# Optimization experiments

Measured on AMD Instinct MI355X. Metric: run time of the kernel, lower is better.

## Reference

```python
import jax, jax.numpy as jnp
import numpy as np

NG, ND = 50000, 20000
EG, ED = 300000, 150000
FG = FD = 256
H = 256
FC = 2048
B = 65536
EPS = 1e-5


def _lrelu(x):
    return jnp.where(x >= 0, x, 0.01 * x)


def _bn(x, g, b):
    # BatchNorm1d in training mode: biased batch stats over the node dim
    m = x.mean(axis=0)
    v = ((x - m) ** 2).mean(axis=0)
    return (x - m) * jax.lax.rsqrt(v + EPS) * g + b


def _gconv(x, edge_index, Wr, br, Ws, n_nodes):
    # PyG GraphConv: out = lin_rel(sum_{j->i} x_j) + lin_root(x_i)
    src, dst = edge_index[0], edge_index[1]
    agg = jax.ops.segment_sum(x[src], dst, num_segments=n_nodes)  # [N, in]
    return agg @ Wr + br + x @ Ws


def setup_inputs() -> dict:
    key = jax.random.key(0)
    ks = iter(jax.random.split(key, 64))
    d = {}
    d["gene_x"] = jax.random.normal(next(ks), (NG, FG), jnp.float32)
    d["disease_x"] = jax.random.normal(next(ks), (ND, FD), jnp.float32)
    d["gene_edge_index"] = jax.random.randint(next(ks), (2, EG), 0, NG, jnp.int32)
    d["disease_edge_index"] = jax.random.randint(next(ks), (2, ED), 0, ND, jnp.int32)
    d["batch_idx"] = jax.random.randint(next(ks), (B, 2), 0, ND, jnp.int32)

    def lin(fin, fout):
        s = 1.0 / np.sqrt(fin)
        W = jax.random.uniform(next(ks), (fin, fout), jnp.float32, -s, s)
        b = jax.random.uniform(next(ks), (fout,), jnp.float32, -s, s)
        return W, b

    for p, fin in (("g", FG), ("d", FD)):
        for i in range(3):
            f = fin if i == 0 else H
            Wr, br = lin(f, H)
            Ws, _ = lin(f, H)
            d[f"{p}{i}_Wr"], d[f"{p}{i}_br"], d[f"{p}{i}_Ws"] = Wr, br, Ws
            d[f"bn{p}{i}_g"] = jnp.ones((H,), jnp.float32)
            d[f"bn{p}{i}_b"] = jnp.zeros((H,), jnp.float32)
    d["lin1_W"], d["lin1_b"] = lin(2 * H, FC)
    d["lin2_W"], d["lin2_b"] = lin(FC, FC // 2)
    d["lin3_W"], d["lin3_b"] = lin(FC // 2, FC // 4)
    d["lin4_W"], d["lin4_b"] = lin(FC // 4, 2)
    return d


def reference(gene_x, disease_x, gene_edge_index, disease_edge_index, batch_idx,
              g0_Wr, g0_br, g0_Ws, g1_Wr, g1_br, g1_Ws, g2_Wr, g2_br, g2_Ws,
              d0_Wr, d0_br, d0_Ws, d1_Wr, d1_br, d1_Ws, d2_Wr, d2_br, d2_Ws,
              bng0_g, bng0_b, bng1_g, bng1_b, bng2_g, bng2_b,
              bnd0_g, bnd0_b, bnd1_g, bnd1_b, bnd2_g, bnd2_b,
              lin1_W, lin1_b, lin2_W, lin2_b, lin3_W, lin3_b, lin4_W, lin4_b):
    # gene tower
    g0 = _bn(_lrelu(_gconv(gene_x, gene_edge_index, g0_Wr, g0_br, g0_Ws, NG)), bng0_g, bng0_b)
    g1 = _bn(_lrelu(_gconv(g0, gene_edge_index, g1_Wr, g1_br, g1_Ws, NG)), bng1_g, bng1_b)
    g2 = _bn(_lrelu(_gconv(g1, gene_edge_index, g2_Wr, g2_br, g2_Ws, NG)), bng2_g, bng2_b)
    gene_out = 0.7 * g0 + 0.2 * g1 + 0.1 * g2
    # disease tower
    h0 = _bn(_lrelu(_gconv(disease_x, disease_edge_index, d0_Wr, d0_br, d0_Ws, ND)), bnd0_g, bnd0_b)
    h1 = _bn(_lrelu(_gconv(h0, disease_edge_index, d1_Wr, d1_br, d1_Ws, ND)), bnd1_g, bnd1_b)
    h2 = _bn(_lrelu(_gconv(h1, disease_edge_index, d2_Wr, d2_br, d2_Ws, ND)), bnd2_g, bnd2_b)
    dis_out = 0.7 * h0 + 0.2 * h1 + 0.1 * h2
    # pair gather + MLP head (dropout is identity in eval)
    x = jnp.concatenate([gene_out[batch_idx[:, 0]], dis_out[batch_idx[:, 1]]], axis=1)
    x = _lrelu(x @ lin1_W + lin1_b)
    x = _lrelu(x @ lin2_W + lin2_b)
    x = _lrelu(x @ lin3_W + lin3_b)
    return x @ lin4_W + lin4_b
```

## Files before the change

kernel.cpp:

```cpp
#include <hip/hip_runtime.h>
#include <hip/hip_bf16.h>
#include <cstdint>
#include <cstddef>

#define N_G 50000
#define N_D 20000
#define E_G 300000
#define E_D 150000
#define BATCH 65536

typedef _Float16 f16;
typedef _Float16 f16x8 __attribute__((ext_vector_type(8)));
typedef _Float16 f16x4 __attribute__((ext_vector_type(4)));
typedef float f32x4 __attribute__((ext_vector_type(4)));

__device__ __forceinline__ float clampf(float v) {
    return fminf(fmaxf(v, -60000.f), 60000.f);
}

__device__ __forceinline__ void gl_lds16(const void* g, void* l) {
    __builtin_amdgcn_global_load_lds(
        (const __attribute__((address_space(1))) unsigned int*)g,
        (__attribute__((address_space(3))) unsigned int*)l, 16, 0, 0);
}

__global__ __launch_bounds__(256) void gemm_f16(
    const f16* __restrict__ A,
    const int* __restrict__ bidx,
    const f16* __restrict__ geneT, const f16* __restrict__ disT, int rowBase,
    const f16* __restrict__ Bt, const float* __restrict__ bias,
    f16* __restrict__ C, int M, int N, int K, int relu, int CB, int RB,
    const float* __restrict__ W4, float* __restrict__ outF)
{
    alignas(16) __shared__ f16 sA[128 * 64];
    alignas(16) __shared__ f16 sB[128 * 64];
    const int t = threadIdx.x;
    const int w = t >> 6, l = t & 63;
    const int wm = w >> 1, wn = w & 1;
    const int q = l >> 4, lr = l & 15;

    int flat = blockIdx.x;
    int cb, rb;
    if ((RB & 7) == 0) {
        int x = flat & 7, idx = flat >> 3;
        int Sx = RB >> 3;
        cb = idx % CB;
        rb = x * Sx + idx / CB;
    } else {
        cb = flat % CB;
        rb = flat / CB;
    }
    const int mBase = rb * 128, nBase = cb * 128;

    const int subrow = l >> 3;
    const int c = l & 7;
    const char* pA[4];
    const char* pD[4];
    const char* pB[4];
    const bool fused = (bidx != nullptr);
    const bool concat = (!fused && disT != nullptr);
    const bool twoSrc = fused || concat;
#pragma unroll
    for (int j = 0; j < 4; j++) {
        int seg = j * 4 + w;
        int lrow = seg * 8 + subrow;
        int coff = ((c ^ (lrow & 7)) << 4);
        if (fused) {
            int rg = rowBase + mBase + lrow;
            int gi = bidx[2 * rg], di = bidx[2 * rg + 1];
            pA[j] = (const char*)geneT + (size_t)gi * 512 + coff;
            pD[j] = (const char*)disT + (size_t)di * 512 + coff;
        } else if (concat) {
            int arow = mBase + lrow; if (arow > M - 1) arow = M - 1;
            pA[j] = (const char*)geneT + (size_t)arow * 512 + coff;
            pD[j] = (const char*)disT + (size_t)arow * 512 + coff;
        } else {
            int arow = mBase + lrow; if (arow > M - 1) arow = M - 1;
            pA[j] = (const char*)A + (size_t)arow * K * 2 + coff;
            pD[j] = nullptr;
        }
        int brow = nBase + lrow; if (brow > N - 1) brow = N - 1;
        pB[j] = (const char*)Bt + (size_t)brow * K * 2 + coff;
    }

    f32x4 acc[4][4] = {};

    for (int k0 = 0; k0 < K; k0 += 64) {
        __syncthreads();
#pragma unroll
        for (int j = 0; j < 4; j++) {
            int seg = j * 4 + w;
            const char* srcA;
            if (twoSrc)
                srcA = (k0 < 256) ? (pA[j] + (size_t)k0 * 2) : (pD[j] + (size_t)(k0 - 256) * 2);
            else
                srcA = pA[j] + (size_t)k0 * 2;
            gl_lds16(srcA, sA + seg * 512);
            gl_lds16(pB[j] + (size_t)k0 * 2, sB + seg * 512);
        }
        __syncthreads();
        f16x8 a0[4], a1[4], b0[4], b1[4];
#pragma unroll
        for (int i = 0; i < 4; i++) {
            int r = wm * 64 + i * 16 + lr;
            int rs = r * 64;
            int x0 = (q ^ (r & 7)) << 3;
            int x1 = ((4 + q) ^ (r & 7)) << 3;
            a0[i] = *(const f16x8*)(sA + rs + x0);
            a1[i] = *(const f16x8*)(sA + rs + x1);
        }
#pragma unroll
        for (int jj = 0; jj < 4; jj++) {
            int r = wn * 64 + jj * 16 + lr;
            int rs = r * 64;
            int x0 = (q ^ (r & 7)) << 3;
            int x1 = ((4 + q) ^ (r & 7)) << 3;
            b0[jj] = *(const f16x8*)(sB + rs + x0);
            b1[jj] = *(const f16x8*)(sB + rs + x1);
        }
#pragma unroll
        for (int i = 0; i < 4; i++)
#pragma unroll
            for (int jj = 0; jj < 4; jj++) {
                acc[i][jj] = __builtin_amdgcn_mfma_f32_16x16x32_f16(a0[i], b0[jj], acc[i][jj], 0, 0, 0);
                acc[i][jj] = __builtin_amdgcn_mfma_f32_16x16x32_f16(a1[i], b1[jj], acc[i][jj], 0, 0, 0);
            }
    }

    if (W4 != nullptr) {
        float w40[4], w41[4];
#pragma unroll
        for (int j = 0; j < 4; j++) {
            int col = nBase + wn * 64 + j * 16 + lr;
            w40[j] = W4[col * 2];
            w41[j] = W4[col * 2 + 1];
        }
#pragma unroll
        for (int i = 0; i < 4; i++) {
#pragma unroll
            for (int r = 0; r < 4; r++) {
                int row = mBase + wm * 64 + i * 16 + q * 4 + r;
                float s0 = 0.f, s1 = 0.f;
#pragma unroll
                for (int j = 0; j < 4; j++) {
                    int col = nBase + wn * 64 + j * 16 + lr;
                    float v = acc[i][j][r] + bias[col];
                    v = v >= 0.f ? v : 0.01f * v;
                    v = clampf(v);
                    s0 += v * w40[j];
                    s1 += v * w41[j];
                }
#pragma unroll
                for (int off = 1; off < 16; off <<= 1) {
                    s0 += __shfl_xor(s0, off);
                    s1 += __shfl_xor(s1, off);
                }
                if (lr == 0 && row < M) {
                    atomicAdd(&outF[(size_t)(rowBase + row) * 2], s0);
                    atomicAdd(&outF[(size_t)(rowBase + row) * 2 + 1], s1);
                }
            }
        }
        return;
    }

    __syncthreads();
    f16* lt = ((w >> 1) ? sB : sA) + (w & 1) * 4096;

    float bj[4];
#pragma unroll
    for (int j = 0; j < 4; j++)
        bj[j] = bias ? bias[nBase + wn * 64 + j * 16 + lr] : 0.f;

#pragma unroll
    for (int i = 0; i < 4; i++)
#pragma unroll
        for (int j = 0; j < 4; j++) {
            int col = j * 16 + lr;
#pragma unroll
            for (int r = 0; r < 4; r++) {
                int row = i * 16 + q * 4 + r;
                float v = acc[i][j][r] + bj[j];
                if (relu) v = v >= 0.f ? v : 0.01f * v;
                v = clampf(v);
                int cs = col ^ ((((row >> 2) & 3) << 4) ^ ((row & 3) << 3));
                lt[row * 64 + cs] = (f16)v;
            }
        }
    __syncthreads();

    const int rr = l >> 3;
    const int c8 = l & 7;
#pragma unroll
    for (int it = 0; it < 8; it++) {
        int row = it * 8 + rr;
        int cs = (c8 * 8) ^ ((((row >> 2) & 3) << 4) ^ ((row & 3) << 3));
        f16x8 vv = *(const f16x8*)(lt + row * 64 + cs);
        int grow = mBase + wm * 64 + row;
        if (grow < M)
            *(f16x8*)(C + (size_t)grow * N + nBase + wn * 64 + c8 * 8) = vv;
    }
}

__global__ __launch_bounds__(512) void gemm_wide(
    const int* __restrict__ bidx,
    const f16* __restrict__ geneT, const f16* __restrict__ disT, int rowBase,
    const f16* __restrict__ Bt, const float* __restrict__ bias,
    f16* __restrict__ C, int M, int N, int K, int CB, int RB)
{
    alignas(16) __shared__ f16 sm[40960];
    f16* const sA = sm;
    f16* const sB = sm + 8192;
    const int t = threadIdx.x;
    const int w = t >> 6, l = t & 63;
    const int q = l >> 4, lr = l & 15;
    const int subrow = l >> 3, c = l & 7;

    int flat = blockIdx.x;
    int cb, rb;
    if ((RB & 7) == 0) {
        int x = flat & 7, idx = flat >> 3;
        int Sx = RB >> 3;
        cb = idx % CB;
        rb = x * Sx + idx / CB;
    } else {
        cb = flat % CB;
        rb = flat / CB;
    }
    const int mBase = rb * 128, nBase = cb * 512;

    const char* pA[2];
    const char* pD[2];
#pragma unroll
    for (int j = 0; j < 2; j++) {
        int row = (w * 2 + j) * 8 + subrow;
        int coff = ((c ^ (row & 7)) << 4);
        int rg = rowBase + mBase + row;
        int gi = bidx[2 * rg], di = bidx[2 * rg + 1];
        pA[j] = (const char*)geneT + (size_t)gi * 512 + coff;
        pD[j] = (const char*)disT + (size_t)di * 512 + coff;
    }
    const char* pB[8];
#pragma unroll
    for (int jj = 0; jj < 8; jj++) {
        int row = (jj * 8 + w) * 8 + subrow;
        int coff = ((c ^ (row & 7)) << 4);
        int brow = nBase + row; if (brow > N - 1) brow = N - 1;
        pB[jj] = (const char*)Bt + (size_t)brow * K * 2 + coff;
    }

    f32x4 acc[8][4] = {};

    for (int k0 = 0; k0 < K; k0 += 64) {
        __syncthreads();
#pragma unroll
        for (int j = 0; j < 2; j++) {
            const char* srcA = (k0 < 256) ? (pA[j] + (size_t)k0 * 2)
                                          : (pD[j] + (size_t)(k0 - 256) * 2);
            gl_lds16(srcA, sA + (w * 2 + j) * 512);
        }
#pragma unroll
        for (int jj = 0; jj < 8; jj++)
            gl_lds16(pB[jj] + (size_t)k0 * 2, sB + (jj * 8 + w) * 512);
        __syncthreads();
#pragma unroll
        for (int ks = 0; ks < 2; ks++) {
            f16x8 bf[4];
#pragma unroll
            for (int nf = 0; nf < 4; nf++) {
                int rB = w * 64 + nf * 16 + lr;
                bf[nf] = *(const f16x8*)(sB + rB * 64 + ((((ks << 2) + q) ^ (rB & 7)) << 3));
            }
#pragma unroll
            for (int mf = 0; mf < 8; mf++) {
                int rA = mf * 16 + lr;
                f16x8 af = *(const f16x8*)(sA + rA * 64 + ((((ks << 2) + q) ^ (rA & 7)) << 3));
#pragma unroll
                for (int nf = 0; nf < 4; nf++)
                    acc[mf][nf] = __builtin_amdgcn_mfma_f32_16x16x32_f16(af, bf[nf], acc[mf][nf], 0, 0, 0);
            }
        }
    }

    f16* lt = sm + w * 4096;
    float bj[4];
#pragma unroll
    for (int nf = 0; nf < 4; nf++)
        bj[nf] = bias[nBase + w * 64 + nf * 16 + lr];

    const int rr = l >> 3;
    const int c8 = l & 7;
#pragma unroll
    for (int half = 0; half < 2; half++) {
        __syncthreads();
#pragma unroll
        for (int mh = 0; mh < 4; mh++) {
            int mf = half * 4 + mh;
#pragma unroll
            for (int nf = 0; nf < 4; nf++) {
                int col = nf * 16 + lr;
#pragma unroll
                for (int r = 0; r < 4; r++) {
                    int row = mh * 16 + q * 4 + r;
                    float v = acc[mf][nf][r] + bj[nf];
                    v = v >= 0.f ? v : 0.01f * v;
                    v = clampf(v);
                    int cs = col ^ ((((row >> 2) & 3) << 4) ^ ((row & 3) << 3));
                    lt[row * 64 + cs] = (f16)v;
                }
            }
        }
        __syncthreads();
#pragma unroll
        for (int it = 0; it < 8; it++) {
            int row = it * 8 + rr;
            int cs = (c8 * 8) ^ ((((row >> 2) & 3) << 4) ^ ((row & 3) << 3));
            f16x8 vv = *(const f16x8*)(lt + row * 64 + cs);
            int grow = mBase + half * 64 + row;
            if (grow < M)
                *(f16x8*)(C + (size_t)grow * N + nBase + w * 64 + c8 * 8) = vv;
        }
    }
}

__global__ __launch_bounds__(256) void gemm_tower2(
    const f16* __restrict__ Xg, const f16* __restrict__ XAg,
    const f16* __restrict__ Btg, const float* __restrict__ biasg,
    f16* __restrict__ Cg, int Mg, int RBg, float* __restrict__ statsg,
    const f16* __restrict__ Xd, const f16* __restrict__ XAd,
    const f16* __restrict__ Btd, const float* __restrict__ biasd,
    f16* __restrict__ Cd, int Md, int RBd, float* __restrict__ statsd)
{
    alignas(16) __shared__ f16 sA[128 * 64];
    alignas(16) __shared__ f16 sB[128 * 64];
    const int t = threadIdx.x;
    const int w = t >> 6, l = t & 63;
    const int wm = w >> 1, wn = w & 1;
    const int q = l >> 4, lr = l & 15;

    int flat = blockIdx.x;
    const int geneBlocks = 2 * RBg;
    const f16* X;  const f16* XA;  const f16* Bt;  const float* bias;
    f16* C;  int M, RB;  float* stats;
    if (flat < geneBlocks) {
        X = Xg; XA = XAg; Bt = Btg; bias = biasg; C = Cg; M = Mg; RB = RBg; stats = statsg;
    } else {
        flat -= geneBlocks;
        X = Xd; XA = XAd; Bt = Btd; bias = biasd; C = Cd; M = Md; RB = RBd; stats = statsd;
    }

    int cb, rb;
    if ((RB & 7) == 0) {
        int x = flat & 7, idx = flat >> 3;
        int Sx = RB >> 3;
        cb = idx % 2;
        rb = x * Sx + idx / 2;
    } else {
        cb = flat % 2;
        rb = flat / 2;
    }
    const int mBase = rb * 128, nBase = cb * 128;

    const int subrow = l >> 3;
    const int c = l & 7;
    const char* pA[4];
    const char* pD[4];
    const char* pB[4];
#pragma unroll
    for (int j = 0; j < 4; j++) {
        int seg = j * 4 + w;
        int lrow = seg * 8 + subrow;
        int coff = ((c ^ (lrow & 7)) << 4);
        int arow = mBase + lrow; if (arow > M - 1) arow = M - 1;
        pA[j] = (const char*)X + (size_t)arow * 512 + coff;
        pD[j] = (const char*)XA + (size_t)arow * 512 + coff;
        int brow = nBase + lrow; if (brow > 255) brow = 255;
        pB[j] = (const char*)Bt + (size_t)brow * 1024 + coff;
    }

    f32x4 acc[4][4] = {};

    for (int k0 = 0; k0 < 512; k0 += 64) {
        __syncthreads();
#pragma unroll
        for (int j = 0; j < 4; j++) {
            int seg = j * 4 + w;
            const char* srcA = (k0 < 256) ? (pA[j] + (size_t)k0 * 2)
                                          : (pD[j] + (size_t)(k0 - 256) * 2);
            gl_lds16(srcA, sA + seg * 512);
            gl_lds16(pB[j] + (size_t)k0 * 2, sB + seg * 512);
        }
        __syncthreads();
        f16x8 a0[4], a1[4], b0[4], b1[4];
#pragma unroll
        for (int i = 0; i < 4; i++) {
            int r = wm * 64 + i * 16 + lr;
            int rs = r * 64;
            int x0 = (q ^ (r & 7)) << 3;
            int x1 = ((4 + q) ^ (r & 7)) << 3;
            a0[i] = *(const f16x8*)(sA + rs + x0);
            a1[i] = *(const f16x8*)(sA + rs + x1);
        }
#pragma unroll
        for (int jj = 0; jj < 4; jj++) {
            int r = wn * 64 + jj * 16 + lr;
            int rs = r * 64;
            int x0 = (q ^ (r & 7)) << 3;
            int x1 = ((4 + q) ^ (r & 7)) << 3;
            b0[jj] = *(const f16x8*)(sB + rs + x0);
            b1[jj] = *(const f16x8*)(sB + rs + x1);
        }
#pragma unroll
        for (int i = 0; i < 4; i++)
#pragma unroll
            for (int jj = 0; jj < 4; jj++) {
                acc[i][jj] = __builtin_amdgcn_mfma_f32_16x16x32_f16(a0[i], b0[jj], acc[i][jj], 0, 0, 0);
                acc[i][jj] = __builtin_amdgcn_mfma_f32_16x16x32_f16(a1[i], b1[jj], acc[i][jj], 0, 0, 0);
            }
    }

    __syncthreads();
    f16* lt = ((w >> 1) ? sB : sA) + (w & 1) * 4096;

    float bj[4];
#pragma unroll
    for (int j = 0; j < 4; j++)
        bj[j] = bias[nBase + wn * 64 + j * 16 + lr];

    float sj[4] = {0.f, 0.f, 0.f, 0.f}, s2j[4] = {0.f, 0.f, 0.f, 0.f};
#pragma unroll
    for (int i = 0; i < 4; i++)
#pragma unroll
        for (int j = 0; j < 4; j++) {
            int col = j * 16 + lr;
#pragma unroll
            for (int r = 0; r < 4; r++) {
                int row = i * 16 + q * 4 + r;
                float v = acc[i][j][r] + bj[j];
                v = v >= 0.f ? v : 0.01f * v;
                v = clampf(v);
                if ((mBase + wm * 64 + row) < M) { sj[j] += v; s2j[j] += v * v; }
                int cs = col ^ ((((row >> 2) & 3) << 4) ^ ((row & 3) << 3));
                lt[row * 64 + cs] = (f16)v;
            }
        }

#pragma unroll
    for (int j = 0; j < 4; j++) {
        float s = sj[j], s2 = s2j[j];
        s += __shfl_xor(s, 16); s2 += __shfl_xor(s2, 16);
        s += __shfl_xor(s, 32); s2 += __shfl_xor(s2, 32);
        if (q == 0) {
            int col = nBase + wn * 64 + j * 16 + lr;
            atomicAdd(&stats[col], s);
            atomicAdd(&stats[256 + col], s2);
        }
    }
    __syncthreads();

    const int rr = l >> 3;
    const int c8 = l & 7;
#pragma unroll
    for (int it = 0; it < 8; it++) {
        int row = it * 8 + rr;
        int cs = (c8 * 8) ^ ((((row >> 2) & 3) << 4) ^ ((row & 3) << 3));
        f16x8 vv = *(const f16x8*)(lt + row * 64 + cs);
        int grow = mBase + wm * 64 + row;
        if (grow < M)
            *(f16x8*)(C + (size_t)grow * 256 + nBase + wn * 64 + c8 * 8) = vv;
    }
}

__global__ void cvt2(const float* __restrict__ gx, const float* __restrict__ dx,
                     f16* __restrict__ og, f16* __restrict__ od) {
    size_t i = ((size_t)blockIdx.x * 256 + threadIdx.x) * 8;
    const size_t ng = (size_t)N_G * 256;
    const float* in; f16* out;
    if (i < ng) { in = gx + i; out = og + i; }
    else {
        size_t j = i - ng;
        if (j >= (size_t)N_D * 256) return;
        in = dx + j; out = od + j;
    }
    f32x4 a = *(const f32x4*)in;
    f32x4 b = *(const f32x4*)(in + 4);
    f16x8 o;
    o[0] = (f16)clampf(a.x); o[1] = (f16)clampf(a.y);
    o[2] = (f16)clampf(a.z); o[3] = (f16)clampf(a.w);
    o[4] = (f16)clampf(b.x); o[5] = (f16)clampf(b.y);
    o[6] = (f16)clampf(b.z); o[7] = (f16)clampf(b.w);
    *(f16x8*)out = o;
}

__global__ void init_out(const float* __restrict__ b4, float* __restrict__ out, int n) {
    int i = blockIdx.x * 256 + threadIdx.x;
    if (i < n) out[i] = b4[i & 1];
}

__global__ void count_deg2(const int* __restrict__ gei, const int* __restrict__ dei,
                           int* __restrict__ cntg, int* __restrict__ cntd) {
    int e = blockIdx.x * 256 + threadIdx.x;
    if (e < E_G) atomicAdd(&cntg[gei[E_G + e]], 1);
    else if (e < E_G + E_D) atomicAdd(&cntd[dei[E_D + (e - E_G)]], 1);
}

__global__ void scan_deg2(const int* __restrict__ cntg, int* __restrict__ rpg,
                          const int* __restrict__ cntd, int* __restrict__ rpd) {
    __shared__ int part[1024];
    const int t = threadIdx.x;
    const int* deg = blockIdx.x ? cntd : cntg;
    int* rowptr = blockIdx.x ? rpd : rpg;
    const int Nn = blockIdx.x ? N_D : N_G;
    const int C = (Nn + 1023) >> 10;
    const int base = t * C;
    int s = 0;
    for (int i = 0; i < C; i++) { int idx = base + i; if (idx < Nn) s += deg[idx]; }
    part[t] = s;
    __syncthreads();
    for (int off = 1; off < 1024; off <<= 1) {
        int v = (t >= off) ? part[t - off] : 0;
        __syncthreads();
        part[t] += v;
        __syncthreads();
    }
    int pre = (t == 0) ? 0 : part[t - 1];
    for (int i = 0; i < C; i++) {
        int idx = base + i;
        if (idx < Nn) { rowptr[idx] = pre; pre += deg[idx]; }
    }
    if (t == 1023) rowptr[Nn] = part[1023];
}

__global__ void fill_csr2(const int* __restrict__ gei, const int* __restrict__ dei,
                          const int* __restrict__ rpg, const int* __restrict__ rpd,
                          int* __restrict__ curg, int* __restrict__ curd,
                          int* __restrict__ csrg, int* __restrict__ csrd) {
    int e = blockIdx.x * 256 + threadIdx.x;
    if (e < E_G) {
        int d = gei[E_G + e];
        int p = rpg[d] + atomicAdd(&curg[d], 1);
        csrg[p] = gei[e];
    } else if (e < E_G + E_D) {
        int e2 = e - E_G;
        int d = dei[E_D + e2];
        int p = rpd[d] + atomicAdd(&curd[d], 1);
        csrd[p] = dei[e2];
    }
}

__global__ void agg_x2(const int* __restrict__ rpg, const int* __restrict__ csrg,
                       const f16* __restrict__ Xg, f16* __restrict__ XAg,
                       const int* __restrict__ rpd, const int* __restrict__ csrd,
                       const f16* __restrict__ Xd, f16* __restrict__ XAd) {
    int gid = blockIdx.x * 256 + threadIdx.x;
    int node = gid >> 6, l = gid & 63;
    const int* rowptr; const int* csr; const f16* X; f16* XA;
    if (node < N_G) { rowptr = rpg; csr = csrg; X = Xg; XA = XAg; }
    else {
        node -= N_G;
        if (node >= N_D) return;
        rowptr = rpd; csr = csrd; X = Xd; XA = XAd;
    }
    int beg = rowptr[node], end = rowptr[node + 1];
    float s0 = 0.f, s1 = 0.f, s2 = 0.f, s3 = 0.f;
    for (int e = beg; e < end; e++) {
        int src = csr[e];
        f16x4 xv = *(const f16x4*)(X + (size_t)src * 256 + l * 4);
        s0 += (float)xv.x; s1 += (float)xv.y; s2 += (float)xv.z; s3 += (float)xv.w;
    }
    f16x4 o;
    o.x = (f16)clampf(s0); o.y = (f16)clampf(s1);
    o.z = (f16)clampf(s2); o.w = (f16)clampf(s3);
    *(f16x4*)(XA + (size_t)node * 256 + l * 4) = o;
}

__global__ void bn_apply2(f16* __restrict__ yg, f16* __restrict__ yd,
                          const float* __restrict__ stg, const float* __restrict__ std_,
                          const float* __restrict__ gg, const float* __restrict__ bg,
                          const float* __restrict__ gd, const float* __restrict__ bd,
                          float invNg, float invNd, float wv,
                          f16* __restrict__ accg, f16* __restrict__ accd, int initAcc) {
    size_t i = ((size_t)blockIdx.x * 256 + threadIdx.x) * 8;
    const size_t ng = (size_t)N_G * 256;
    f16* y; f16* acc; const float* stats; const float* g; const float* b; float invN;
    if (i < ng) { y = yg + i; acc = accg + i; stats = stg; g = gg; b = bg; invN = invNg; }
    else {
        size_t j = i - ng;
        if (j >= (size_t)N_D * 256) return;
        y = yd + j; acc = accd + j; stats = std_; g = gd; b = bd; invN = invNd;
    }
    int colb = (int)(i & 255);
    f16x8 yv = *(const f16x8*)y;
    f16x8 av = {};
    if (!initAcc) av = *(const f16x8*)acc;
    f16x8 yo, ao;
#pragma unroll
    for (int j = 0; j < 8; j++) {
        int col = colb + j;
        float m = stats[col] * invN;
        float var = stats[256 + col] * invN - m * m;
        if (var < 0.f) var = 0.f;
        float rs = 1.0f / sqrtf(var + 1e-5f);
        float v = ((float)yv[j] - m) * rs * g[col] + b[col];
        v = clampf(v);
        yo[j] = (f16)v;
        float p = initAcc ? 0.f : (float)av[j];
        ao[j] = (f16)clampf(p + wv * v);
    }
    *(f16x8*)y = yo;
    *(f16x8*)acc = ao;
}

__global__ void transpose_tile(const float* __restrict__ W, f16* __restrict__ WT,
                               int K, int N, int dstRowOff, int dstColOff, int LK) {
    __shared__ float tile[32][33];
    int n0 = blockIdx.x * 32, k0 = blockIdx.y * 32;
    int tx = threadIdx.x, ty = threadIdx.y;
    for (int yy = ty; yy < 32; yy += 8) {
        int k = k0 + yy, n = n0 + tx;
        tile[yy][tx] = (k < K && n < N) ? W[(size_t)k * N + n] : 0.f;
    }
    __syncthreads();
    for (int yy = ty; yy < 32; yy += 8) {
        int n = n0 + yy, k = k0 + tx;
        if (n < N && k < K)
            WT[(size_t)(dstRowOff + n) * LK + dstColOff + k] = (f16)clampf(tile[tx][yy]);
    }
}

struct WPtrs { const float* p[12]; };
__global__ void transpose12(WPtrs wp, f16* __restrict__ WT) {
    __shared__ float tile[32][33];
    const int z = blockIdx.z;
    const float* W = wp.p[z];
    const int s = z >> 1;
    const int colOff = (z & 1) * 256;
    f16* dst = WT + (size_t)s * 131072;
    int n0 = blockIdx.x * 32, k0 = blockIdx.y * 32;
    int tx = threadIdx.x, ty = threadIdx.y;
    for (int yy = ty; yy < 32; yy += 8)
        tile[yy][tx] = W[(size_t)(k0 + yy) * 256 + n0 + tx];
    __syncthreads();
    for (int yy = ty; yy < 32; yy += 8)
        dst[(size_t)(n0 + yy) * 512 + colOff + k0 + tx] = (f16)clampf(tile[tx][yy]);
}

extern "C" void kernel_launch(void* const* d_in, const int* in_sizes, int n_in,
                              void* d_out, int out_size, void* d_ws, size_t ws_size,
                              hipStream_t stream) {
    char* ws = (char*)d_ws;
    size_t off = 0;
    auto alloc = [&](size_t bytes) -> void* {
        void* p = ws + off;
        off += (bytes + 255) & ~(size_t)255;
        return p;
    };

    f16* gene_out = (f16*)alloc((size_t)N_G * 256 * 2);
    f16* dis_out  = (f16*)alloc((size_t)N_D * 256 * 2);
    f16* W1T = (f16*)alloc((size_t)2048 * 512 * 2);
    f16* W2T = (f16*)alloc((size_t)1024 * 2048 * 2);
    f16* W3T = (f16*)alloc((size_t)512 * 1024 * 2);
    f16* WcatT = (f16*)alloc((size_t)6 * 256 * 512 * 2);
    int* csr_g = (int*)alloc((size_t)E_G * 4);
    int* csr_d = (int*)alloc((size_t)E_D * 4);
    int* rp_g = (int*)alloc((size_t)(N_G + 1) * 4);
    int* rp_d = (int*)alloc((size_t)(N_D + 1) * 4);
    int* cnt = (int*)alloc((size_t)(N_G + N_D) * 4);
    int* cnt_g = cnt;
    int* cnt_d = cnt + N_G;
    float* statsAll = (float*)alloc(6 * 512 * 4);

    char* scratch = ws + off;
    size_t avail = (ws_size > off) ? (ws_size - off) : 0;

    const size_t NSG = (size_t)N_G * 256;
    const size_t NSD = (size_t)N_D * 256;
    f16* gX = (f16*)scratch;
    f16* gY = gX + NSG;
    f16* gXA = gY + NSG;
    f16* dX = gXA + NSG;
    f16* dY = dX + NSD;
    f16* dXA = dY + NSD;

    int R = BATCH;
    while ((size_t)R * 6144 > avail && R > 256) R >>= 1;
    int chunks = BATCH / R;
    f16* h1 = (f16*)scratch;
    f16* h2 = h1 + (size_t)R * 2048;

    const float* gene_x = (const float*)d_in[0];
    const float* disease_x = (const float*)d_in[1];
    const int* g_ei = (const int*)d_in[2];
    const int* d_ei = (const int*)d_in[3];
    const int* bidx = (const int*)d_in[4];
    float* out = (float*)d_out;

    const float wl[3] = {0.7f, 0.2f, 0.1f};

    hipMemsetAsync(statsAll, 0, 6 * 512 * 4, stream);
    hipMemsetAsync(cnt, 0, (size_t)(N_G + N_D) * 4, stream);
    {
        size_t tot8 = ((NSG + NSD) / 8 + 255) / 256;
        cvt2<<<(int)tot8, 256, 0, stream>>>(gene_x, disease_x, gX, dX);
    }
    count_deg2<<<(E_G + E_D + 255) / 256, 256, 0, stream>>>(g_ei, d_ei, cnt_g, cnt_d);
    scan_deg2<<<2, 1024, 0, stream>>>(cnt_g, rp_g, cnt_d, rp_d);
    hipMemsetAsync(cnt, 0, (size_t)(N_G + N_D) * 4, stream);
    fill_csr2<<<(E_G + E_D + 255) / 256, 256, 0, stream>>>(g_ei, d_ei, rp_g, rp_d,
                                                           cnt_g, cnt_d, csr_g, csr_d);
    {
        WPtrs wp;
        for (int l = 0; l < 3; l++) {
            wp.p[l * 2 + 0] = (const float*)d_in[5 + l * 5 + 2];
            wp.p[l * 2 + 1] = (const float*)d_in[5 + l * 5 + 0];
            wp.p[6 + l * 2 + 0] = (const float*)d_in[20 + l * 5 + 2];
            wp.p[6 + l * 2 + 1] = (const float*)d_in[20 + l * 5 + 0];
        }
        transpose12<<<dim3(8, 8, 12), dim3(32, 8), 0, stream>>>(wp, WcatT);
    }

    const int RBg = ((N_G + 127) / 128 + 7) & ~7;
    const int RBd = ((N_D + 127) / 128 + 7) & ~7;
    f16* gIn = gX; f16* gOut = gY;
    f16* dIn = dX; f16* dOut = dY;
    int aggBlocks = ((N_G + N_D) * 64 + 255) / 256;
    int bnBlocks = (int)(((NSG + NSD) / 8 + 255) / 256);
    for (int l = 0; l < 3; l++) {
        const float* br_g = (const float*)d_in[5 + l * 5 + 1];
        const float* bg_g = (const float*)d_in[5 + l * 5 + 3];
        const float* bb_g = (const float*)d_in[5 + l * 5 + 4];
        const float* br_d = (const float*)d_in[20 + l * 5 + 1];
        const float* bg_d = (const float*)d_in[20 + l * 5 + 3];
        const float* bb_d = (const float*)d_in[20 + l * 5 + 4];
        agg_x2<<<aggBlocks, 256, 0, stream>>>(rp_g, csr_g, gIn, gXA,
                                              rp_d, csr_d, dIn, dXA);
        gemm_tower2<<<2 * RBg + 2 * RBd, 256, 0, stream>>>(
            gIn, gXA, WcatT + (size_t)l * 131072, br_g, gOut, N_G, RBg, statsAll + l * 512,
            dIn, dXA, WcatT + (size_t)(3 + l) * 131072, br_d, dOut, N_D, RBd,
            statsAll + (3 + l) * 512);
        bn_apply2<<<bnBlocks, 256, 0, stream>>>(gOut, dOut,
                                                statsAll + l * 512, statsAll + (3 + l) * 512,
                                                bg_g, bb_g, bg_d, bb_d,
                                                1.0f / N_G, 1.0f / N_D, wl[l],
                                                gene_out, dis_out, l == 0);
        f16* tmp = gIn; gIn = gOut; gOut = tmp;
        tmp = dIn; dIn = dOut; dOut = tmp;
    }

    const float* lin1_W = (const float*)d_in[35];
    const float* lin1_b = (const float*)d_in[36];
    const float* lin2_W = (const float*)d_in[37];
    const float* lin2_b = (const float*)d_in[38];
    const float* lin3_W = (const float*)d_in[39];
    const float* lin3_b = (const float*)d_in[40];
    const float* lin4_W = (const float*)d_in[41];
    const float* lin4_b = (const float*)d_in[42];

    transpose_tile<<<dim3(64, 16), dim3(32, 8), 0, stream>>>(lin1_W, W1T, 512, 2048, 0, 0, 512);
    transpose_tile<<<dim3(32, 64), dim3(32, 8), 0, stream>>>(lin2_W, W2T, 2048, 1024, 0, 0, 2048);
    transpose_tile<<<dim3(16, 32), dim3(32, 8), 0, stream>>>(lin3_W, W3T, 1024, 512, 0, 0, 1024);
    init_out<<<(BATCH * 2 + 255) / 256, 256, 0, stream>>>(lin4_b, out, BATCH * 2);

    for (int c = 0; c < chunks; c++) {
        int rb = c * R;
        int RB = R / 128;
        if ((R & 127) == 0) {
            gemm_wide<<<4 * RB, 512, 0, stream>>>(bidx, gene_out, dis_out, rb,
                                                  W1T, lin1_b, h1, R, 2048, 512, 4, RB);
        } else {
            gemm_f16<<<16 * RB, 256, 0, stream>>>(nullptr, bidx, gene_out, dis_out, rb,
                                                  W1T, lin1_b, h1, R, 2048, 512, 1, 16, RB,
                                                  nullptr, nullptr);
        }
        gemm_f16<<<8 * RB, 256, 0, stream>>>(h1, nullptr, nullptr, nullptr, 0,
                                             W2T, lin2_b, h2, R, 1024, 2048, 1, 8, RB,
                                             nullptr, nullptr);
        gemm_f16<<<4 * RB, 256, 0, stream>>>(h2, nullptr, nullptr, nullptr, rb,
                                             W3T, lin3_b, nullptr, R, 512, 1024, 1, 4, RB,
                                             lin4_W, out);
    }
}
```

Baseline: 1.378 ms.

## Add 256x256-tile 8-wave pipelined GEMM for lin2 layer

Adds a new 512-thread GEMM kernel with 256x256 output tiles, triple-buffered A and double-buffered B loads staged straight into LDS, interleaved MFMA phases with barriers and priority hints, and an XCD-aware block remap. The lin2 GEMM (2048->1024) uses it when the chunk size is a multiple of 256. The larger tiles raise operand reuse and the prefetch schedule is meant to overlap loads with MFMA work. The cost is fewer, heavier blocks (160KB LDS, many accumulator registers), so occupancy drops.

```diff
diff --git a/kernel.cpp b/kernel.cpp
--- a/kernel.cpp
+++ b/kernel.cpp
@@ -197,6 +197,203 @@
         int cs = (c8 * 8) ^ ((((row >> 2) & 3) << 4) ^ ((row & 3) << 3));
         f16x8 vv = *(const f16x8*)(lt + row * 64 + cs);
         int grow = mBase + wm * 64 + row;
+        if (grow < M)
+            *(f16x8*)(C + (size_t)grow * N + nBase + wn * 64 + c8 * 8) = vv;
+    }
+}
+
+__global__ __launch_bounds__(512) void gemm8p(
+    const f16* __restrict__ A, const f16* __restrict__ Bt,
+    const float* __restrict__ bias, f16* __restrict__ C,
+    int M, int N, int K, int CB, int RB)
+{
+    alignas(16) __shared__ f16 sm[81920];
+    f16* const smA = sm;
+    f16* const smB = sm + 3 * 16384;
+    const int t = threadIdx.x;
+    const int w = t >> 6, l = t & 63;
+    const int wm = w >> 2, wn = w & 3;
+    const int q = l >> 4, lr = l & 15;
+    const int subrow = l >> 3, c = l & 7;
+
+    int flat = blockIdx.x;
+    int cb, rb;
+    if ((RB & 7) == 0) {
+        int x = flat & 7, idx = flat >> 3;
+        int Sx = RB >> 3;
+        cb = idx % CB;
+        rb = x * Sx + idx / CB;
+    } else {
+        cb = flat % CB;
+        rb = flat / CB;
+    }
+    const int mBase = rb * 256, nBase = cb * 256;
+
+    const char* pA[4];
+    const char* pB[4];
+#pragma unroll
+    for (int jj = 0; jj < 4; jj++) {
+        int row = jj * 64 + w * 8 + subrow;
+        int coff = ((c ^ (row & 7)) << 4);
+        int ga = mBase + row; if (ga > M - 1) ga = M - 1;
+        pA[jj] = (const char*)A + (size_t)ga * K * 2 + coff;
+        int gb = nBase + row; if (gb > N - 1) gb = N - 1;
+        pB[jj] = (const char*)Bt + (size_t)gb * K * 2 + coff;
+    }
+
+    auto stA = [&](int buf, int k0, int half) {
+        f16* dst = smA + buf * 16384;
+#pragma unroll
+        for (int j = 0; j < 2; j++) {
+            int jj = half * 2 + j;
+            gl_lds16(pA[jj] + (size_t)k0 * 2, dst + (jj * 64 + w * 8) * 64);
+        }
+    };
+    auto stB = [&](int buf, int k0, int half) {
+        f16* dst = smB + buf * 16384;
+#pragma unroll
+        for (int j = 0; j < 2; j++) {
+            int jj = half * 2 + j;
+            gl_lds16(pB[jj] + (size_t)k0 * 2, dst + (jj * 64 + w * 8) * 64);
+        }
+    };
+
+    f32x4 acc[8][4] = {};
+    const int nkt = K >> 6;
+
+    stA(0, 0, 0); stA(0, 0, 1);
+    stB(0, 0, 0); stB(0, 0, 1);
+    if (nkt > 1) { stA(1, 64, 0); stA(1, 64, 1); }
+    asm volatile("s_waitcnt vmcnt(4)" ::: "memory");
+    __builtin_amdgcn_s_barrier();
+    __builtin_amdgcn_sched_barrier(0);
+
+    for (int kt = 0; kt < nkt; kt++) {
+        const f16* bA = smA + (kt % 3) * 16384;
+        const f16* bB = smB + (kt & 1) * 16384;
+        const int kB1 = (kt + 1) << 6;
+        const int kA2 = (kt + 2) << 6;
+        f16x8 bf[4], af[4];
+
+#pragma unroll
+        for (int nf = 0; nf < 4; nf++) {
+            int rB = wn * 64 + nf * 16 + lr;
+            bf[nf] = *(const f16x8*)(bB + rB * 64 + ((q ^ (rB & 7)) << 3));
+        }
+#pragma unroll
+        for (int mf = 0; mf < 4; mf++) {
+            int rA = wm * 128 + mf * 16 + lr;
+            af[mf] = *(const f16x8*)(bA + rA * 64 + ((q ^ (rA & 7)) << 3));
+        }
+        if (kt + 1 < nkt) stB((kt + 1) & 1, kB1, 0);
+        __builtin_amdgcn_sched_barrier(0);
+        __builtin_amdgcn_s_barrier();
+        __builtin_amdgcn_s_setprio(1);
+#pragma unroll
+        for (int mf = 0; mf < 4; mf++)
+#pragma unroll
+            for (int nf = 0; nf < 4; nf++)
+                acc[mf][nf] = __builtin_amdgcn_mfma_f32_16x16x32_f16(af[mf], bf[nf], acc[mf][nf], 0, 0, 0);
+        __builtin_amdgcn_s_setprio(0);
+        __builtin_amdgcn_sched_barrier(0);
+        __builtin_amdgcn_s_barrier();
+
+#pragma unroll
+        for (int mf = 0; mf < 4; mf++) {
+            int rA = wm * 128 + (mf + 4) * 16 + lr;
+            af[mf] = *(const f16x8*)(bA + rA * 64 + ((q ^ (rA & 7)) << 3));
+        }
+        if (kt + 1 < nkt) stB((kt + 1) & 1, kB1, 1);
+        __builtin_amdgcn_sched_barrier(0);
+        __builtin_amdgcn_s_barrier();
+        __builtin_amdgcn_s_setprio(1);
+#pragma unroll
+        for (int mf = 0; mf < 4; mf++)
+#pragma unroll
+            for (int nf = 0; nf < 4; nf++)
+                acc[mf + 4][nf] = __builtin_amdgcn_mfma_f32_16x16x32_f16(af[mf], bf[nf], acc[mf + 4][nf], 0, 0, 0);
+        __builtin_amdgcn_s_setprio(0);
+        __builtin_amdgcn_sched_barrier(0);
+        __builtin_amdgcn_s_barrier();
+
+#pragma unroll
+        for (int nf = 0; nf < 4; nf++) {
+            int rB = wn * 64 + nf * 16 + lr;
+            bf[nf] = *(const f16x8*)(bB + rB * 64 + (((4 + q) ^ (rB & 7)) << 3));
+        }
+#pragma unroll
+        for (int mf = 0; mf < 4; mf++) {
+            int rA = wm * 128 + mf * 16 + lr;
+            af[mf] = *(const f16x8*)(bA + rA * 64 + (((4 + q) ^ (rA & 7)) << 3));
+        }
+        if (kt + 2 < nkt) stA((kt + 2) % 3, kA2, 0);
+        __builtin_amdgcn_sched_barrier(0);
+        __builtin_amdgcn_s_barrier();
+        __builtin_amdgcn_s_setprio(1);
+#pragma unroll
+        for (int mf = 0; mf < 4; mf++)
+#pragma unroll
+            for (int nf = 0; nf < 4; nf++)
+                acc[mf][nf] = __builtin_amdgcn_mfma_f32_16x16x32_f16(af[mf], bf[nf], acc[mf][nf], 0, 0, 0);
+        __builtin_amdgcn_s_setprio(0);
+        __builtin_amdgcn_sched_barrier(0);
+        __builtin_amdgcn_s_barrier();
+
+#pragma unroll
+        for (int mf = 0; mf < 4; mf++) {
+            int rA = wm * 128 + (mf + 4) * 16 + lr;
+            af[mf] = *(const f16x8*)(bA + rA * 64 + (((4 + q) ^ (rA & 7)) << 3));
+        }
+        if (kt + 2 < nkt) {
+            stA((kt + 2) % 3, kA2, 1);
+            asm volatile("s_waitcnt vmcnt(4)" ::: "memory");
+        } else {
+            asm volatile("s_waitcnt vmcnt(0)" ::: "memory");
+        }
+        __builtin_amdgcn_sched_barrier(0);
+        __builtin_amdgcn_s_barrier();
+        __builtin_amdgcn_s_setprio(1);
+#pragma unroll
+        for (int mf = 0; mf < 4; mf++)
+#pragma unroll
+            for (int nf = 0; nf < 4; nf++)
+                acc[mf + 4][nf] = __builtin_amdgcn_mfma_f32_16x16x32_f16(af[mf], bf[nf], acc[mf + 4][nf], 0, 0, 0);
+        __builtin_amdgcn_s_setprio(0);
+        __builtin_amdgcn_sched_barrier(0);
+        __builtin_amdgcn_s_barrier();
+    }
+    __builtin_amdgcn_sched_barrier(0);
+
+    f16* lt = sm + w * 8192;
+    float bj[4];
+#pragma unroll
+    for (int nf = 0; nf < 4; nf++)
+        bj[nf] = bias[nBase + wn * 64 + nf * 16 + lr];
+
+#pragma unroll
+    for (int mf = 0; mf < 8; mf++)
+#pragma unroll
+        for (int nf = 0; nf < 4; nf++) {
+            int col = nf * 16 + lr;
+#pragma unroll
+            for (int r = 0; r < 4; r++) {
+                int row = mf * 16 + q * 4 + r;
+                float v = acc[mf][nf][r] + bj[nf];
+                v = v >= 0.f ? v : 0.01f * v;
+                v = clampf(v);
+                int cs = col ^ ((((row >> 2) & 3) << 4) ^ ((row & 3) << 3));
+                lt[row * 64 + cs] = (f16)v;
+            }
+        }
+
+    const int rr = l >> 3;
+    const int c8 = l & 7;
+#pragma unroll
+    for (int it = 0; it < 16; it++) {
+        int row = it * 8 + rr;
+        int cs = (c8 * 8) ^ ((((row >> 2) & 3) << 4) ^ ((row & 3) << 3));
+        f16x8 vv = *(const f16x8*)(lt + row * 64 + cs);
+        int grow = mBase + wm * 128 + row;
         if (grow < M)
             *(f16x8*)(C + (size_t)grow * N + nBase + wn * 64 + c8 * 8) = vv;
     }
@@ -773,9 +970,14 @@
                                                   W1T, lin1_b, h1, R, 2048, 512, 1, 16, RB,
                                                   nullptr, nullptr);
         }
-        gemm_f16<<<8 * RB, 256, 0, stream>>>(h1, nullptr, nullptr, nullptr, 0,
-                                             W2T, lin2_b, h2, R, 1024, 2048, 1, 8, RB,
-                                             nullptr, nullptr);
+        if ((R & 255) == 0) {
+            int RB2 = R / 256;
+            gemm8p<<<4 * RB2, 512, 0, stream>>>(h1, W2T, lin2_b, h2, R, 1024, 2048, 4, RB2);
+        } else {
+            gemm_f16<<<8 * RB, 256, 0, stream>>>(h1, nullptr, nullptr, nullptr, 0,
+                                                 W2T, lin2_b, h2, R, 1024, 2048, 1, 8, RB,
+                                                 nullptr, nullptr);
+        }
         gemm_f16<<<4 * RB, 256, 0, stream>>>(h2, nullptr, nullptr, nullptr, rb,
                                              W3T, lin3_b, nullptr, R, 512, 1024, 1, 4, RB,
                                              lin4_W, out);
```

Measured after the change: 1.317 ms. 4.4% less time.
